# Kernel optimization log

Hardware: AMD Instinct MI355X
Metric: run time of the kernel (lower is better)

## Reference

```python
import jax, jax.numpy as jnp
import numpy as np

GRID = (32, 32)          # 448 // 14
IMG = (448, 448)
SIGMA = 4.0              # anomalib AnomalyMapGenerator default smoothing


def _l2norm(x, axis=-1, eps=1e-12):
    return x / jnp.clip(jnp.linalg.norm(x, axis=axis, keepdims=True), eps, None)


def _gaussian_blur(x, sigma=SIGMA):
    # kornia-style: kernel_size = 2*int(4*sigma+0.5)+1, reflect padding, separable conv
    radius = int(4.0 * sigma + 0.5)
    t = jnp.arange(-radius, radius + 1, dtype=x.dtype)
    k = jnp.exp(-0.5 * (t / sigma) ** 2)
    k = k / k.sum()
    xp = jnp.pad(x, ((0, 0), (0, 0), (radius, radius), (radius, radius)), mode='reflect')
    kh = k.reshape(1, 1, -1, 1)
    kw = k.reshape(1, 1, 1, -1)
    dn = ('NCHW', 'OIHW', 'NCHW')
    y = jax.lax.conv_general_dilated(xp, kh, (1, 1), 'VALID', dimension_numbers=dn)
    return jax.lax.conv_general_dilated(y, kw, (1, 1), 'VALID', dimension_numbers=dn)


def setup_inputs() -> dict:
    key = jax.random.key(0)
    k1, k2 = jax.random.split(key)
    features = jax.random.normal(k1, (8, 1024, 384), dtype=jnp.float32)
    memory_bank = jax.random.normal(k2, (65536, 384), dtype=jnp.float32)
    return {"features": features, "memory_bank": memory_bank}


def reference(features, memory_bank):
    # features: (B, N, D) patch tokens from DINOv2; memory_bank: (M, D)
    b, n, _ = features.shape
    f = _l2norm(features)                 # F.normalize(features, p=2, dim=1) on flattened patches
    mb = _l2norm(memory_bank)             # bank stores normalized embeddings
    sim = jnp.einsum('bnd,md->bnm', f, mb)            # (B, N, M) cosine similarity
    dists = jnp.clip(1.0 - sim, 0.0, 2.0)
    min_dists = dists.min(axis=2)                     # k = num_neighbours = 1 -> row min
    num_top = max(int(n * 0.01), 1)
    top_vals = jax.lax.top_k(min_dists, num_top)[0]
    pred_score = top_vals.mean(axis=1, keepdims=True) # (B, 1)
    amap = min_dists.reshape(b, 1, *GRID)
    amap = jax.image.resize(amap, (b, 1, *IMG), method='bilinear')
    anomaly_map = _gaussian_blur(amap)                # (B, 1, H, W)
    return pred_score, anomaly_map
```

## Files before the change

kernel.cpp:

```cpp
#include <hip/hip_runtime.h>
#include <hip/hip_bf16.h>

#define NROW_F 8192
#define NROW_B 65536
#define KDIM   384
#define BM 128
#define BN 256
#define NSUB 8
#define NGRP (NROW_B / (BN * NSUB))
#define NBM  (NROW_F / BM)
#define NWG  (NBM * NGRP)

#define LDSA 0
#define LDSB 49152
#define LDSR 49152
#define LDS_TOT 81920

typedef int   i32x4 __attribute__((ext_vector_type(4)));
typedef float f32x4 __attribute__((ext_vector_type(4)));

static __device__ __forceinline__ void stage16(const void* g, void* l) {
  __builtin_amdgcn_global_load_lds(
      (const __attribute__((address_space(1))) unsigned int*)g,
      (__attribute__((address_space(3))) unsigned int*)l, 16, 0, 0);
}

__global__ __launch_bounds__(256) void quantize_rows_kernel(
    const float* __restrict__ in, char* __restrict__ out8,
    float* __restrict__ scales, int nrows) {
  int row  = blockIdx.x * 4 + (threadIdx.x >> 6);
  int lane = threadIdx.x & 63;
  if (row >= nrows) return;
  const float* r = in + (size_t)row * KDIM;
  float v[6];
  float ss = 0.f, mx = 0.f;
#pragma unroll
  for (int i = 0; i < 6; ++i) {
    v[i] = r[lane + i * 64];
    ss += v[i] * v[i];
    mx = fmaxf(mx, fabsf(v[i]));
  }
#pragma unroll
  for (int d = 1; d < 64; d <<= 1) {
    ss += __shfl_xor(ss, d, 64);
    mx = fmaxf(mx, __shfl_xor(mx, d, 64));
  }
  mx = fmaxf(mx, 1e-30f);
  float inv = rsqrtf(fmaxf(ss, 1e-24f));
  float scl = 127.0f / mx;
  if (lane == 0) scales[row] = mx * inv * (1.0f / 127.0f);
  char* o = out8 + (size_t)row * KDIM;
#pragma unroll
  for (int i = 0; i < 6; ++i)
    o[lane + i * 64] = (char)__float2int_rn(v[i] * scl);
}

__global__ __launch_bounds__(256, 2) void maxsim_kernel(
    const char* __restrict__ F8,
    const char* __restrict__ B8,
    const float* __restrict__ sA,
    const float* __restrict__ sB,
    float* __restrict__ partial) {
  __shared__ __align__(16) char smem[LDS_TOT];

  const int tid  = threadIdx.x;
  const int wv   = tid >> 6;
  const int lane = tid & 63;
  const int l15  = lane & 15;
  const int lhi  = lane >> 4;
  const int wr   = wv >> 1;
  const int wc   = wv & 1;

  const int wg  = (blockIdx.x & 7) * (NWG / 8) + (blockIdx.x >> 3);
  const int bm  = wg & (NBM - 1);
  const int grp = wg >> 6;
  const size_t brow = (size_t)bm * BM;

  const int srow = tid >> 2;
  const int gsw  = (tid & 3) ^ ((tid >> 3) & 3);

  {
    const char* gA = F8 + (size_t)(brow + srow) * KDIM + gsw * 16;
    char* lA = smem + LDSA + wv * 1024;
#pragma unroll
    for (int kt = 0; kt < 6; ++kt) {
      stage16(gA + kt * 64,             lA + kt * 8192);
      stage16(gA + kt * 64 + 64 * KDIM, lA + kt * 8192 + 4096);
    }
  }

  auto stageB = [&](int s2, int koff, int buf) {
    const char* g = B8 + ((size_t)grp * 2048 + s2 * 256 + srow) * KDIM
                    + koff * 64 + gsw * 16;
    char* l = smem + LDSB + buf * 16384 + wv * 1024;
#pragma unroll
    for (int j = 0; j < 4; ++j)
      stage16(g + (size_t)(j * 64) * KDIM, l + j * 4096);
  };
  stageB(0, 0, 0);
  stageB(0, 1, 1);

  const int cof = ((l15 >> 1) & 3) << 4;

  auto ldA8 = [&](int k6, int m) -> i32x4 {
    int byte = k6 * 8192 + (wr * 64 + m * 16 + l15) * 64 + ((lhi << 4) ^ cof);
    return *reinterpret_cast<const i32x4*>(smem + LDSA + byte);
  };
  auto ldB8 = [&](int buf, int n) -> i32x4 {
    int byte = buf * 16384 + (wc * 128 + n * 16 + l15) * 64 + ((lhi << 4) ^ cof);
    return *reinterpret_cast<const i32x4*>(smem + LDSB + byte);
  };

  i32x4 acc[4][8];
  f32x4 vm[4];
#pragma unroll
  for (int m = 0; m < 4; ++m) {
    vm[m] = f32x4{-1e30f, -1e30f, -1e30f, -1e30f};
#pragma unroll
    for (int n = 0; n < 8; ++n) acc[m][n] = i32x4{0, 0, 0, 0};
  }

  asm volatile("s_waitcnt vmcnt(4)" ::: "memory");
  __builtin_amdgcn_s_barrier();

  for (int sub = 0; sub < NSUB; ++sub) {
#pragma unroll
    for (int k6 = 0; k6 < 6; ++k6) {
      i32x4 a[4], b[8];
#pragma unroll
      for (int m = 0; m < 4; ++m) a[m] = ldA8(k6, m);
#pragma unroll
      for (int n = 0; n < 8; ++n) b[n] = ldB8(k6 & 1, n);
      asm volatile("s_waitcnt lgkmcnt(0)" ::: "memory");
      __builtin_amdgcn_sched_barrier(0);
      __builtin_amdgcn_s_barrier();

      {
        const int s2   = (k6 < 4) ? sub : ((sub + 1) & 7);
        const int koff = (k6 + 2) % 6;
        stageB(s2, koff, k6 & 1);
      }
      __builtin_amdgcn_s_setprio(1);
#pragma unroll
      for (int n = 0; n < 8; ++n)
#pragma unroll
        for (int m = 0; m < 4; ++m)
          acc[m][n] = __builtin_amdgcn_mfma_i32_16x16x64_i8(
              a[m], b[n], acc[m][n], 0, 0, 0);
      __builtin_amdgcn_s_setprio(0);
      asm volatile("s_waitcnt vmcnt(4)" ::: "memory");
      __builtin_amdgcn_s_barrier();
    }
    const float* sbp = sB + (size_t)grp * 2048 + sub * 256 + wc * 128 + l15;
    float sb[8];
#pragma unroll
    for (int n = 0; n < 8; ++n) sb[n] = sbp[n * 16];
#pragma unroll
    for (int m = 0; m < 4; ++m) {
#pragma unroll
      for (int n = 0; n < 8; ++n)
#pragma unroll
        for (int j = 0; j < 4; ++j)
          vm[m][j] = fmaxf(vm[m][j], (float)acc[m][n][j] * sb[n]);
#pragma unroll
      for (int n = 0; n < 8; ++n) acc[m][n] = i32x4{0, 0, 0, 0};
    }
  }

  asm volatile("s_waitcnt vmcnt(0)" ::: "memory");
  __syncthreads();
#pragma unroll
  for (int d = 1; d < 16; d <<= 1)
#pragma unroll
    for (int m = 0; m < 4; ++m)
#pragma unroll
      for (int j = 0; j < 4; ++j)
        vm[m][j] = fmaxf(vm[m][j], __shfl_xor(vm[m][j], d, 64));

  float* red = (float*)(smem + LDSR);
  if (l15 == 0) {
#pragma unroll
    for (int m = 0; m < 4; ++m)
#pragma unroll
      for (int j = 0; j < 4; ++j)
        red[wc * 128 + wr * 64 + m * 16 + lhi * 4 + j] = vm[m][j];
  }
  __syncthreads();
  if (tid < BM) {
    float x = fmaxf(red[tid], red[128 + tid]);
    partial[(size_t)grp * NROW_F + brow + tid] = x * sA[brow + tid];
  }
}

__global__ __launch_bounds__(256) void combine_kernel(
    const float* __restrict__ partial, float* __restrict__ md) {
  int r = blockIdx.x * 256 + threadIdx.x;
  if (r >= NROW_F) return;
  float m = -1e30f;
#pragma unroll
  for (int c = 0; c < NGRP; ++c) m = fmaxf(m, partial[(size_t)c * NROW_F + r]);
  float d = 1.0f - m;
  d = fminf(fmaxf(d, 0.0f), 2.0f);
  md[r] = d;
}

__global__ __launch_bounds__(256) void topk_kernel(
    const float* __restrict__ md, float* __restrict__ out) {
  __shared__ float buf[1024];
  __shared__ float svals[256];
  __shared__ int   sidx[256];
  int b = blockIdx.x, tid = threadIdx.x;
  for (int i = tid; i < 1024; i += 256) buf[i] = md[b * 1024 + i];
  __syncthreads();
  float total = 0.f;
  for (int it = 0; it < 10; ++it) {
    float best = -1e30f; int bi = 0;
    for (int i = tid; i < 1024; i += 256)
      if (buf[i] > best) { best = buf[i]; bi = i; }
    svals[tid] = best; sidx[tid] = bi;
    __syncthreads();
    for (int s = 128; s > 0; s >>= 1) {
      if (tid < s && svals[tid + s] > svals[tid]) {
        svals[tid] = svals[tid + s]; sidx[tid] = sidx[tid + s];
      }
      __syncthreads();
    }
    if (tid == 0) { total += svals[0]; buf[sidx[0]] = -1e30f; }
    __syncthreads();
  }
  if (tid == 0) out[b] = total * 0.1f;
}

__global__ __launch_bounds__(256) void build_w_kernel(float* __restrict__ W) {
  int idx = blockIdx.x * 256 + threadIdx.x;
  if (idx >= 448 * 32) return;
  int y = idx >> 5, g = idx & 31;
  float ksum = 0.f, acc = 0.f;
#pragma unroll
  for (int t = -16; t <= 16; ++t) {
    float ft = (float)t * 0.25f;
    float kv = expf(-0.5f * ft * ft);
    ksum += kv;
    int p = y + t;
    p = (p < 0) ? -p : ((p > 447) ? 894 - p : p);
    float src = ((float)p + 0.5f) * (1.0f / 14.0f) - 0.5f;
    float fl = floorf(src);
    int i0 = (int)fl;
    float fr = src - fl;
    int c0 = i0 < 0 ? 0 : (i0 > 31 ? 31 : i0);
    int i1 = i0 + 1;
    int c1 = i1 < 0 ? 0 : (i1 > 31 ? 31 : i1);
    float w = 0.f;
    if (c0 == g) w += 1.0f - fr;
    if (c1 == g) w += fr;
    acc += kv * w;
  }
  W[idx] = acc / ksum;
}

__global__ __launch_bounds__(256) void map_stage1_kernel(
    const float* __restrict__ md, const float* __restrict__ W,
    float* __restrict__ tmp) {
  int idx = blockIdx.x * 256 + threadIdx.x;
  if (idx >= 8 * 448 * 32) return;
  int gx = idx & 31;
  int y  = (idx >> 5) % 448;
  int b  = idx / (448 * 32);
  const float* w = W + y * 32;
  const float* m = md + b * 1024 + gx;
  float s = 0.f;
#pragma unroll
  for (int gy = 0; gy < 32; ++gy) s += w[gy] * m[gy * 32];
  tmp[idx] = s;
}

__global__ __launch_bounds__(256) void map_stage2_kernel(
    const float* __restrict__ tmp, const float* __restrict__ W,
    float* __restrict__ out) {
  int idx = blockIdx.x * 256 + threadIdx.x;
  if (idx >= 8 * 448 * 448) return;
  int x    = idx % 448;
  int ypos = idx / 448;
  const float* w = W + x * 32;
  const float* t = tmp + ypos * 32;
  float s = 0.f;
#pragma unroll
  for (int gx = 0; gx < 32; ++gx) s += w[gx] * t[gx];
  out[idx] = s;
}

extern "C" void kernel_launch(void* const* d_in, const int* in_sizes, int n_in,
                              void* d_out, int out_size, void* d_ws, size_t ws_size,
                              hipStream_t stream) {
  const float* features = (const float*)d_in[0];
  const float* bank     = (const float*)d_in[1];
  float* out = (float*)d_out;

  char* ws = (char*)d_ws;
  char*  mb8     = ws;
  char*  f8      = ws + 25165824;
  float* sB      = (float*)(ws + 28311552);
  float* sA      = (float*)(ws + 28573696);
  float* partial = (float*)(ws + 28606464);
  float* md      = (float*)(ws + 29655040);
  float* W       = (float*)(ws + 29687808);
  float* tmp     = (float*)(ws + 29745152);

  quantize_rows_kernel<<<NROW_B / 4, 256, 0, stream>>>(bank, mb8, sB, NROW_B);
  quantize_rows_kernel<<<NROW_F / 4, 256, 0, stream>>>(features, f8, sA, NROW_F);
  maxsim_kernel<<<NWG, 256, 0, stream>>>(f8, mb8, sA, sB, partial);
  combine_kernel<<<NROW_F / 256, 256, 0, stream>>>(partial, md);
  topk_kernel<<<8, 256, 0, stream>>>(md, out);
  build_w_kernel<<<(448 * 32 + 255) / 256, 256, 0, stream>>>(W);
  map_stage1_kernel<<<(8 * 448 * 32 + 255) / 256, 256, 0, stream>>>(md, W, tmp);
  map_stage2_kernel<<<(8 * 448 * 448 + 255) / 256, 256, 0, stream>>>(tmp, W, out + 8);
}
```

Baseline: 259.4 us.

## Halve B tile, double-buffer register fragments, stage bank scales into LDS

Shrinks the memory-bank tile from 256 to 128 rows per sub-step, doubling the number of sub-steps and halving the accumulator registers. LDS fragment loads for the next k-slice are now issued in ping-pong register sets before the MFMAs on the current slice, so LDS latency is meant to overlap with compute. Per-row bank scales are also prefetched into LDS once instead of being read from global memory after each sub-step. In exchange each barrier now covers half as many MFMAs and waits for all outstanding global loads (vmcnt(0)), which may expose more load latency and synchronisation.

Result: no change. 257.7 us (-0.7%).

```diff
diff --git a/kernel.cpp b/kernel.cpp
--- a/kernel.cpp
+++ b/kernel.cpp
@@ -5,16 +5,17 @@
 #define NROW_B 65536
 #define KDIM   384
 #define BM 128
-#define BN 256
-#define NSUB 8
+#define BN 128
+#define NSUB 16
 #define NGRP (NROW_B / (BN * NSUB))
 #define NBM  (NROW_F / BM)
 #define NWG  (NBM * NGRP)
 
 #define LDSA 0
 #define LDSB 49152
+#define LDSS 65536
 #define LDSR 49152
-#define LDS_TOT 81920
+#define LDS_TOT 73728
 
 typedef int   i32x4 __attribute__((ext_vector_type(4)));
 typedef float f32x4 __attribute__((ext_vector_type(4)));
@@ -88,14 +89,18 @@
       stage16(gA + kt * 64 + 64 * KDIM, lA + kt * 8192 + 4096);
     }
   }
+  {
+    const char* gs = (const char*)(sB + (size_t)grp * 2048) + tid * 16;
+    stage16(gs,        smem + LDSS + wv * 1024);
+    stage16(gs + 4096, smem + LDSS + 4096 + wv * 1024);
+  }
 
   auto stageB = [&](int s2, int koff, int buf) {
-    const char* g = B8 + ((size_t)grp * 2048 + s2 * 256 + srow) * KDIM
+    const char* g = B8 + ((size_t)grp * 2048 + s2 * 128 + srow) * KDIM
                     + koff * 64 + gsw * 16;
-    char* l = smem + LDSB + buf * 16384 + wv * 1024;
-#pragma unroll
-    for (int j = 0; j < 4; ++j)
-      stage16(g + (size_t)(j * 64) * KDIM, l + j * 4096);
+    char* l = smem + LDSB + buf * 8192 + wv * 1024;
+    stage16(g, l);
+    stage16(g + (size_t)64 * KDIM, l + 4096);
   };
   stageB(0, 0, 0);
   stageB(0, 1, 1);
@@ -107,68 +112,80 @@
     return *reinterpret_cast<const i32x4*>(smem + LDSA + byte);
   };
   auto ldB8 = [&](int buf, int n) -> i32x4 {
-    int byte = buf * 16384 + (wc * 128 + n * 16 + l15) * 64 + ((lhi << 4) ^ cof);
+    int byte = buf * 8192 + (wc * 64 + n * 16 + l15) * 64 + ((lhi << 4) ^ cof);
     return *reinterpret_cast<const i32x4*>(smem + LDSB + byte);
   };
 
-  i32x4 acc[4][8];
+  i32x4 acc[4][4];
   f32x4 vm[4];
 #pragma unroll
   for (int m = 0; m < 4; ++m) {
     vm[m] = f32x4{-1e30f, -1e30f, -1e30f, -1e30f};
 #pragma unroll
-    for (int n = 0; n < 8; ++n) acc[m][n] = i32x4{0, 0, 0, 0};
-  }
-
-  asm volatile("s_waitcnt vmcnt(4)" ::: "memory");
+    for (int n = 0; n < 4; ++n) acc[m][n] = i32x4{0, 0, 0, 0};
+  }
+
+  asm volatile("s_waitcnt vmcnt(2)" ::: "memory");
   __builtin_amdgcn_s_barrier();
 
+  i32x4 aA[4], bA[4], aB[4], bB[4];
+#pragma unroll
+  for (int m = 0; m < 4; ++m) aA[m] = ldA8(0, m);
+#pragma unroll
+  for (int n = 0; n < 4; ++n) bA[n] = ldB8(0, n);
+  asm volatile("s_waitcnt lgkmcnt(0)" ::: "memory");
+
+#define PHASE(K6, AC, BC, AN, BN_) do {                                       \
+    asm volatile("s_waitcnt vmcnt(0)" ::: "memory");   \
+    __builtin_amdgcn_s_barrier();                      \
+    __builtin_amdgcn_sched_barrier(0);                                        \
+    _Pragma("unroll")                                                         \
+    for (int m = 0; m < 4; ++m) AN[m] = ldA8(((K6) + 1) % 6, m);              \
+    _Pragma("unroll")                                                         \
+    for (int n = 0; n < 4; ++n) BN_[n] = ldB8(((K6) + 1) & 1, n);             \
+    {                                                                         \
+      const int s2 = ((K6) < 4) ? sub : ((sub + 1) & (NSUB - 1));             \
+      stageB(s2, ((K6) + 2) % 6, (K6) & 1);                                   \
+    }                                                                         \
+    __builtin_amdgcn_sched_barrier(0);                                        \
+    __builtin_amdgcn_s_setprio(1);                                            \
+    _Pragma("unroll")                                                         \
+    for (int n = 0; n < 4; ++n)                                               \
+      _Pragma("unroll")                                                       \
+      for (int m = 0; m < 4; ++m)                                             \
+        acc[m][n] = __builtin_amdgcn_mfma_i32_16x16x64_i8(                    \
+            AC[m], BC[n], acc[m][n], 0, 0, 0);                                \
+    __builtin_amdgcn_s_setprio(0);                                            \
+    asm volatile("s_waitcnt lgkmcnt(0)" ::: "memory");                        \
+    __builtin_amdgcn_sched_barrier(0);                                        \
+  } while (0)
+
   for (int sub = 0; sub < NSUB; ++sub) {
-#pragma unroll
-    for (int k6 = 0; k6 < 6; ++k6) {
-      i32x4 a[4], b[8];
-#pragma unroll
-      for (int m = 0; m < 4; ++m) a[m] = ldA8(k6, m);
-#pragma unroll
-      for (int n = 0; n < 8; ++n) b[n] = ldB8(k6 & 1, n);
-      asm volatile("s_waitcnt lgkmcnt(0)" ::: "memory");
-      __builtin_amdgcn_sched_barrier(0);
-      __builtin_amdgcn_s_barrier();
-
-      {
-        const int s2   = (k6 < 4) ? sub : ((sub + 1) & 7);
-        const int koff = (k6 + 2) % 6;
-        stageB(s2, koff, k6 & 1);
-      }
-      __builtin_amdgcn_s_setprio(1);
-#pragma unroll
-      for (int n = 0; n < 8; ++n)
-#pragma unroll
-        for (int m = 0; m < 4; ++m)
-          acc[m][n] = __builtin_amdgcn_mfma_i32_16x16x64_i8(
-              a[m], b[n], acc[m][n], 0, 0, 0);
-      __builtin_amdgcn_s_setprio(0);
-      asm volatile("s_waitcnt vmcnt(4)" ::: "memory");
-      __builtin_amdgcn_s_barrier();
-    }
-    const float* sbp = sB + (size_t)grp * 2048 + sub * 256 + wc * 128 + l15;
-    float sb[8];
-#pragma unroll
-    for (int n = 0; n < 8; ++n) sb[n] = sbp[n * 16];
+    PHASE(0, aA, bA, aB, bB);
+    PHASE(1, aB, bB, aA, bA);
+    PHASE(2, aA, bA, aB, bB);
+    PHASE(3, aB, bB, aA, bA);
+    PHASE(4, aA, bA, aB, bB);
+    PHASE(5, aB, bB, aA, bA);
+    float sb[4];
+#pragma unroll
+    for (int n = 0; n < 4; ++n)
+      sb[n] = *reinterpret_cast<const float*>(
+          smem + LDSS + (sub * 128 + wc * 64 + n * 16 + l15) * 4);
 #pragma unroll
     for (int m = 0; m < 4; ++m) {
 #pragma unroll
-      for (int n = 0; n < 8; ++n)
+      for (int n = 0; n < 4; ++n)
 #pragma unroll
         for (int j = 0; j < 4; ++j)
           vm[m][j] = fmaxf(vm[m][j], (float)acc[m][n][j] * sb[n]);
 #pragma unroll
-      for (int n = 0; n < 8; ++n) acc[m][n] = i32x4{0, 0, 0, 0};
+      for (int n = 0; n < 4; ++n) acc[m][n] = i32x4{0, 0, 0, 0};
     }
   }
+#undef PHASE
 
   asm volatile("s_waitcnt vmcnt(0)" ::: "memory");
-  __syncthreads();
 #pragma unroll
   for (int d = 1; d < 16; d <<= 1)
 #pragma unroll
@@ -178,6 +195,7 @@
         vm[m][j] = fmaxf(vm[m][j], __shfl_xor(vm[m][j], d, 64));
 
   float* red = (float*)(smem + LDSR);
+  __syncthreads();
   if (l15 == 0) {
 #pragma unroll
     for (int m = 0; m < 4; ++m)
```
